# Performance work log

Measured on AMD Instinct MI355X. Metric: run time of the kernel, lower is better.

## Reference

```python
import jax, jax.numpy as jnp
import numpy as np

NB_HEAD = 16
SIZE_PER_HEAD = 64
D_MODEL = 1024
B, S = 4, 2048
NEG_BIG = 1e12  # matches the 1e12 additive-mask constant in the original


def setup_inputs() -> dict:
    key = jax.random.key(0)
    ks = jax.random.split(key, 8)
    Q_seq = jax.random.normal(ks[0], (B, S, D_MODEL), dtype=jnp.float32)
    K_seq = jax.random.normal(ks[1], (B, S, D_MODEL), dtype=jnp.float32)
    V_seq = jax.random.normal(ks[2], (B, S, D_MODEL), dtype=jnp.float32)
    out_dim = NB_HEAD * SIZE_PER_HEAD
    # glorot_uniform-style init
    lim = float(np.sqrt(6.0 / (D_MODEL + out_dim)))
    WQ = jax.random.uniform(ks[3], (D_MODEL, out_dim), minval=-lim, maxval=lim, dtype=jnp.float32)
    WK = jax.random.uniform(ks[4], (D_MODEL, out_dim), minval=-lim, maxval=lim, dtype=jnp.float32)
    WV = jax.random.uniform(ks[5], (D_MODEL, out_dim), minval=-lim, maxval=lim, dtype=jnp.float32)
    Q_len = jax.random.randint(ks[6], (B, 1), 1, S + 1, dtype=jnp.int32)
    V_len = jax.random.randint(ks[7], (B, 1), 1, S + 1, dtype=jnp.int32)
    return {"Q_seq": Q_seq, "K_seq": K_seq, "V_seq": V_seq,
            "WQ": WQ, "WK": WK, "WV": WV, "Q_len": Q_len, "V_len": V_len}


def _len_mask(lengths, seqlen, dtype):
    # one_hot(L) then 1 - cumsum along seq == (pos < L); L >= seqlen -> all ones
    return (jnp.arange(seqlen)[None, :] < lengths[:, 0][:, None]).astype(dtype)


def reference(Q_seq, K_seq, V_seq, WQ, WK, WV, Q_len, V_len):
    b, s, _ = Q_seq.shape
    h, dh = NB_HEAD, SIZE_PER_HEAD
    q = (Q_seq @ WQ).reshape(b, s, h, dh).transpose(0, 2, 1, 3)  # [B,H,S,Dh]
    k = (K_seq @ WK).reshape(b, s, h, dh).transpose(0, 2, 1, 3)
    v = (V_seq @ WV).reshape(b, s, h, dh).transpose(0, 2, 1, 3)
    scores = jnp.einsum('bhqd,bhkd->bhqk', q, k) / jnp.sqrt(jnp.float32(dh))
    mask_k = _len_mask(V_len, s, scores.dtype)  # [B,Sk]
    scores = scores - (1.0 - mask_k)[:, None, None, :] * NEG_BIG
    A = jax.nn.softmax(scores, axis=-1)
    o = jnp.einsum('bhqk,bhkd->bhqd', A, v)
    o = o.transpose(0, 2, 1, 3).reshape(b, s, h * dh)  # [B,S,D]
    mask_q = _len_mask(Q_len, s, o.dtype)
    return o * mask_q[:, :, None]
```

## Files before the change

kernel.cpp:

```cpp
#include <hip/hip_runtime.h>
#include <stdint.h>

typedef __attribute__((ext_vector_type(4))) float f32x4;
typedef __attribute__((ext_vector_type(8))) short bf16x8;
typedef __attribute__((ext_vector_type(4))) unsigned short u16x4;

#define MFMA16(a, b, c) __builtin_amdgcn_mfma_f32_16x16x32_bf16((a), (b), (c), 0, 0, 0)

static __device__ __forceinline__ unsigned short f2bf(float x) {
  union { float f; unsigned int u; } v; v.f = x;
  unsigned int r = v.u + 0x7fffu + ((v.u >> 16) & 1u);
  return (unsigned short)(r >> 16);
}

static __device__ __forceinline__ void gload_lds16(const void* g, void* l) {
  __builtin_amdgcn_global_load_lds(
      (__attribute__((address_space(1))) void*)(g),
      (__attribute__((address_space(3))) void*)(l), 16, 0, 0);
}

template <int CTRL>
static __device__ __forceinline__ float dpp_mov(float x) {
  union { float f; int i; } u, r;
  u.f = x;
  r.i = __builtin_amdgcn_update_dpp(u.i, u.i, CTRL, 0xF, 0xF, false);
  return r.f;
}
static __device__ __forceinline__ float dpp_max16(float x) {
  x = fmaxf(x, dpp_mov<0xB1>(x));
  x = fmaxf(x, dpp_mov<0x4E>(x));
  x = fmaxf(x, dpp_mov<0x124>(x));
  x = fmaxf(x, dpp_mov<0x128>(x));
  return x;
}
static __device__ __forceinline__ float dpp_sum16(float x) {
  x += dpp_mov<0xB1>(x);
  x += dpp_mov<0x4E>(x);
  x += dpp_mov<0x124>(x);
  x += dpp_mov<0x128>(x);
  return x;
}

__global__ void fill_kernel(float* p, int n, float v) {
  int i = blockIdx.x * blockDim.x + threadIdx.x;
  if (i < n) p[i] = v;
}

__global__ __launch_bounds__(256) void conv3_kernel(
    const float* __restrict__ S0, const float* __restrict__ S1, const float* __restrict__ S2,
    unsigned short* __restrict__ D0, unsigned short* __restrict__ D1,
    unsigned short* __restrict__ D2,
    const int* __restrict__ Qlen, const int* __restrict__ Vlen)
{
  const int y = blockIdx.y;
  {
    const int m0 = blockIdx.x * 4;
    const int b = m0 >> 11, s0 = m0 & 2047;
    const int L = (y == 0) ? Qlen[b] : Vlen[b];
    if (s0 >= ((L + 63) & ~63)) return;
  }
  const float* in = (y == 0) ? S0 : (y == 1) ? S1 : S2;
  unsigned short* outp = (y == 0) ? D0 : (y == 1) ? D1 : D2;
  const size_t base = ((size_t)blockIdx.x * 256 + threadIdx.x) * 16;
  const f32x4 a0 = *(const f32x4*)&in[base];
  const f32x4 a1 = *(const f32x4*)&in[base + 4];
  const f32x4 a2 = *(const f32x4*)&in[base + 8];
  const f32x4 a3 = *(const f32x4*)&in[base + 12];
  bf16x8 p0, p1;
#pragma unroll
  for (int u = 0; u < 4; ++u) {
    p0[u]     = (short)f2bf(a0[u]);
    p0[u + 4] = (short)f2bf(a1[u]);
    p1[u]     = (short)f2bf(a2[u]);
    p1[u + 4] = (short)f2bf(a3[u]);
  }
  *(bf16x8*)&outp[base]     = p0;
  *(bf16x8*)&outp[base + 8] = p1;
}

__global__ __launch_bounds__(256) void conv_kernel(
    const float* __restrict__ in, unsigned short* __restrict__ outp)
{
  const size_t base = ((size_t)blockIdx.x * 256 + threadIdx.x) * 16;
  const f32x4 a0 = *(const f32x4*)&in[base];
  const f32x4 a1 = *(const f32x4*)&in[base + 4];
  const f32x4 a2 = *(const f32x4*)&in[base + 8];
  const f32x4 a3 = *(const f32x4*)&in[base + 12];
  bf16x8 p0, p1;
#pragma unroll
  for (int u = 0; u < 4; ++u) {
    p0[u]     = (short)f2bf(a0[u]);
    p0[u + 4] = (short)f2bf(a1[u]);
    p1[u]     = (short)f2bf(a2[u]);
    p1[u + 4] = (short)f2bf(a3[u]);
  }
  *(bf16x8*)&outp[base]     = p0;
  *(bf16x8*)&outp[base + 8] = p1;
}

__global__ __launch_bounds__(256) void wtrans_kernel(
    const float* __restrict__ W0, const float* __restrict__ W1, const float* __restrict__ W2,
    unsigned short* __restrict__ T0, unsigned short* __restrict__ T1, unsigned short* __restrict__ T2)
{
  __shared__ __align__(16) float tile[64][65];
  const float* W = (blockIdx.z == 0) ? W0 : (blockIdx.z == 1) ? W1 : W2;
  unsigned short* T = (blockIdx.z == 0) ? T0 : (blockIdx.z == 1) ? T1 : T2;
  const int t = threadIdx.x;
  const int kb = blockIdx.x * 64, nb = blockIdx.y * 64;
  const int rr = t >> 4, cc = (t & 15) * 4;
#pragma unroll
  for (int p = 0; p < 4; ++p) {
    const int r = rr + p * 16;
    const f32x4 v = *(const f32x4*)&W[(size_t)(kb + r) * 1024 + nb + cc];
#pragma unroll
    for (int j = 0; j < 4; ++j) tile[r][cc + j] = v[j];
  }
  __syncthreads();
#pragma unroll
  for (int p = 0; p < 4; ++p) {
    const int n = rr + p * 16;
    u16x4 o;
#pragma unroll
    for (int j = 0; j < 4; ++j) o[j] = f2bf(tile[cc + j][n]);
    *(u16x4*)&T[(size_t)(nb + n) * 1024 + kb + cc] = o;
  }
}

__global__ __launch_bounds__(256) void proj_gemm_kernel(
    const unsigned short* __restrict__ A0, const unsigned short* __restrict__ A1,
    const unsigned short* __restrict__ A2,
    const unsigned short* __restrict__ B0, const unsigned short* __restrict__ B1,
    const unsigned short* __restrict__ B2,
    unsigned short* __restrict__ O0, unsigned short* __restrict__ O1,
    unsigned short* __restrict__ O2, int zbase,
    const int* __restrict__ Qlen, const int* __restrict__ Vlen)
{
  const int z = blockIdx.z + zbase;
  const int mm = (blockIdx.x + 8 * blockIdx.y + 24 * z) & 63;
  const int m0 = mm * 128, n0 = blockIdx.y * 128;

  int glim;
  {
    const int b = m0 >> 11, s0 = m0 & 2047;
    const int L = (z == 0) ? Qlen[b] : Vlen[b];
    const int C = (L + 63) & ~63;
    if (s0 >= C) return;
    glim = (m0 - s0) + C;
  }

  const unsigned short* Ab = (z == 0) ? A0 : (z == 1) ? A1 : A2;
  const unsigned short* Bt = (z == 0) ? B0 : (z == 1) ? B1 : B2;
  unsigned short* outp = (z == 0) ? O0 : (z == 1) ? O1 : O2;
  const float scale = (z == 0) ? 0.125f : 1.0f;

  __shared__ __align__(16) unsigned short Alds[4][128 * 32];
  __shared__ __align__(16) unsigned short Blds[4][128 * 32];
  const int t = threadIdx.x;
  const int lane = t & 63, w = t >> 6;
  const int wr = w >> 1, wc = w & 1;

  f32x4 acc[4][4] = {};

  const int L0 = t, L1 = t + 256;
  const int r0 = L0 >> 2, c0 = ((L0 & 3) ^ ((r0 >> 1) & 3)) * 8;
  const int r1 = L1 >> 2, c1 = ((L1 & 3) ^ ((r1 >> 1) & 3)) * 8;
  const int ra0 = min(m0 + r0, glim - 1);
  const int ra1 = min(m0 + r1, glim - 1);

#define PROJ_STAGE(tile, buf)                                                        \
  do {                                                                               \
    const int kt_ = (tile) * 32;                                                     \
    gload_lds16(&Ab[(size_t)ra0 * 1024 + kt_ + c0], &Alds[(buf)][L0 * 8]);           \
    gload_lds16(&Bt[(size_t)(n0 + r0) * 1024 + kt_ + c0], &Blds[(buf)][L0 * 8]);     \
    gload_lds16(&Ab[(size_t)ra1 * 1024 + kt_ + c1], &Alds[(buf)][L1 * 8]);           \
    gload_lds16(&Bt[(size_t)(n0 + r1) * 1024 + kt_ + c1], &Blds[(buf)][L1 * 8]);     \
  } while (0)

  PROJ_STAGE(0, 0);
  PROJ_STAGE(1, 1);
  PROJ_STAGE(2, 2);
  asm volatile("s_waitcnt vmcnt(8)" ::: "memory");
  __builtin_amdgcn_s_barrier();
  __builtin_amdgcn_sched_barrier(0);

  for (int tt = 0; tt < 32; ++tt) {
    const int cur = tt & 3;
    if (tt + 3 < 32) PROJ_STAGE(tt + 3, (tt + 3) & 3);

    const int q = lane >> 4;
    bf16x8 af[4], bfv[4];
#pragma unroll
    for (int m = 0; m < 4; ++m) {
      const int row = wr * 64 + m * 16 + (lane & 15);
      af[m] = *(const bf16x8*)&Alds[cur][row * 32 + ((q ^ ((row >> 1) & 3)) * 8)];
    }
#pragma unroll
    for (int n = 0; n < 4; ++n) {
      const int row = wc * 64 + n * 16 + (lane & 15);
      bfv[n] = *(const bf16x8*)&Blds[cur][row * 32 + ((q ^ ((row >> 1) & 3)) * 8)];
    }
    __builtin_amdgcn_s_setprio(1);
#pragma unroll
    for (int m = 0; m < 4; ++m)
#pragma unroll
      for (int n = 0; n < 4; ++n)
        acc[m][n] = MFMA16(af[m], bfv[n], acc[m][n]);
    __builtin_amdgcn_s_setprio(0);

    if (tt < 29)       asm volatile("s_waitcnt vmcnt(8)" ::: "memory");
    else if (tt == 29) asm volatile("s_waitcnt vmcnt(4)" ::: "memory");
    else               asm volatile("s_waitcnt vmcnt(0)" ::: "memory");
    __builtin_amdgcn_s_barrier();
    __builtin_amdgcn_sched_barrier(0);
  }
#undef PROJ_STAGE

#pragma unroll
  for (int mi = 0; mi < 4; ++mi) {
#pragma unroll
    for (int ni = 0; ni < 4; ++ni) {
      const int nn = n0 + wc * 64 + ni * 16 + (lane & 15);
      const int h = nn >> 6, d = nn & 63;
      const int mbase = m0 + wr * 64 + mi * 16 + ((lane >> 4) << 2);
      const int b = mbase >> 11;
      const int s = mbase & 2047;
      if (z != 2) {
#pragma unroll
        for (int j = 0; j < 4; ++j)
          outp[((size_t)(b * 16 + h) * 2048 + (s + j)) * 64 + d] = f2bf(acc[mi][ni][j] * scale);
      } else {
        u16x4 o;
#pragma unroll
        for (int j = 0; j < 4; ++j) o[j] = f2bf(acc[mi][ni][j]);
        *(u16x4*)&outp[((size_t)(b * 16 + h) * 64 + d) * 2048 + s] = o;
      }
    }
  }
}

__global__ __launch_bounds__(256) void attn_kernel(
    const unsigned short* __restrict__ qa, const unsigned short* __restrict__ ka,
    const unsigned short* __restrict__ va, const int* __restrict__ Qlen,
    const int* __restrict__ Vlen, float* __restrict__ outp)
{
  __shared__ __align__(16) unsigned char smem[36864];
  const int t = threadIdx.x, lane = t & 63, w = t >> 6;
  const int bh = blockIdx.y, b = bh >> 4, h = bh & 15;
  const int q0 = blockIdx.x * 16;
  const int Lq = Qlen[b], Lv = Vlen[b];
  float* outb = outp + (size_t)b * 2048 * 1024 + h * 64;

  if (q0 >= Lq) {
    const int r = t >> 4, c0 = (t & 15) * 4;
    const f32x4 z = {0.f, 0.f, 0.f, 0.f};
    *(f32x4*)&outb[(size_t)(q0 + r) * 1024 + c0] = z;
    return;
  }

  const unsigned short* qb = qa + (size_t)bh * 2048 * 64;
  const unsigned short* kb = ka + (size_t)bh * 2048 * 64;
  const unsigned short* vb = va + (size_t)bh * 64 * 2048;

  unsigned short* Klds = (unsigned short*)(smem + w * 9216);
  unsigned short* Vlds = (unsigned short*)(smem + w * 9216 + 4096);
  unsigned short* Plds = (unsigned short*)(smem + w * 9216 + 8192);

  bf16x8 aq[2];
  {
    const int qrow = q0 + (lane & 15);
#pragma unroll
    for (int f = 0; f < 2; ++f)
      aq[f] = *(const bf16x8*)&qb[(size_t)qrow * 64 + (lane >> 4) * 8 + f * 32];
  }

  float m_run[4], l_run[4];
  f32x4 acc_o[4] = {};
#pragma unroll
  for (int j = 0; j < 4; ++j) { m_run[j] = -3.0e38f; l_run[j] = 0.0f; }

  const int nt = (Lv + 31) >> 5;

  bf16x8 krg[4], vrg[4];
  int kt = w;
  if (kt < nt) {
    const int k0 = kt * 32;
#pragma unroll
    for (int i = 0; i < 4; ++i) {
      const int ci = lane + i * 64;
      krg[i] = *(const bf16x8*)&kb[(size_t)(k0 + (ci >> 3)) * 64 + (ci & 7) * 8];
      vrg[i] = *(const bf16x8*)&vb[(size_t)(ci >> 2) * 2048 + k0 + (ci & 3) * 8];
    }
#pragma unroll
    for (int i = 0; i < 4; ++i) {
      const int ci = lane + i * 64;
      const int kr = ci >> 3, kc = ci & 7;
      const int vr = ci >> 2, vc = ci & 3;
      *(bf16x8*)&Klds[kr * 64 + ((kc ^ (kr & 7)) * 8)] = krg[i];
      *(bf16x8*)&Vlds[vr * 32 + ((vc ^ (vr & 3)) * 8)] = vrg[i];
    }
  }

  for (; kt < nt; kt += 4) {
    const int k0 = kt * 32;
    const bool more = (kt + 4) < nt;
    if (more) {
      const int kn = k0 + 128;
#pragma unroll
      for (int i = 0; i < 4; ++i) {
        const int ci = lane + i * 64;
        krg[i] = *(const bf16x8*)&kb[(size_t)(kn + (ci >> 3)) * 64 + (ci & 7) * 8];
        vrg[i] = *(const bf16x8*)&vb[(size_t)(ci >> 2) * 2048 + kn + (ci & 3) * 8];
      }
    }

    f32x4 s4[2];
    __builtin_amdgcn_s_setprio(1);
#pragma unroll
    for (int kbk = 0; kbk < 2; ++kbk) {
      const int row = kbk * 16 + (lane & 15);
      f32x4 acc = {0.f, 0.f, 0.f, 0.f};
#pragma unroll
      for (int ds = 0; ds < 2; ++ds) {
        const int col = (((lane >> 4) * 8) + ds * 32) ^ ((row & 7) << 3);
        const bf16x8 bk = *(const bf16x8*)&Klds[row * 64 + col];
        acc = MFMA16(aq[ds], bk, acc);
      }
      if (k0 + row >= Lv) {
#pragma unroll
        for (int j = 0; j < 4; ++j) acc[j] = -1e30f;
      }
      s4[kbk] = acc;
    }
    __builtin_amdgcn_s_setprio(0);

    float mn[4], esc[4];
#pragma unroll
    for (int j = 0; j < 4; ++j) {
      float rm = fmaxf(s4[0][j], s4[1][j]);
      rm = dpp_max16(rm);
      mn[j] = fmaxf(m_run[j], rm);
      esc[j] = __expf(m_run[j] - mn[j]);
      m_run[j] = mn[j];
    }

    float p[2][4];
    float rs[4] = {0.f, 0.f, 0.f, 0.f};
#pragma unroll
    for (int kbk = 0; kbk < 2; ++kbk)
#pragma unroll
      for (int j = 0; j < 4; ++j) {
        p[kbk][j] = __expf(s4[kbk][j] - mn[j]);
        rs[j] += p[kbk][j];
      }

#pragma unroll
    for (int kbk = 0; kbk < 2; ++kbk)
#pragma unroll
      for (int j = 0; j < 4; ++j) {
        const int row = (lane >> 4) * 4 + j;
        const int pcol = kbk * 16 + (lane & 15);
        Plds[row * 32 + (((pcol >> 3) ^ (row & 3)) * 8) + (pcol & 7)] = f2bf(p[kbk][j]);
      }

#pragma unroll
    for (int j = 0; j < 4; ++j) {
      const float s = dpp_sum16(rs[j]);
      l_run[j] = l_run[j] * esc[j] + s;
    }
#pragma unroll
    for (int d = 0; d < 4; ++d)
#pragma unroll
      for (int j = 0; j < 4; ++j) acc_o[d][j] *= esc[j];

    bf16x8 pf;
    {
      const int row = lane & 15;
      pf = *(const bf16x8*)&Plds[row * 32 + (((lane >> 4) ^ (row & 3)) * 8)];
    }

    __builtin_amdgcn_s_setprio(1);
#pragma unroll
    for (int db = 0; db < 4; ++db) {
      const int vrow = db * 16 + (lane & 15);
      const int vch = (lane >> 4) ^ (vrow & 3);
      const bf16x8 vf = *(const bf16x8*)&Vlds[vrow * 32 + vch * 8];
      acc_o[db] = MFMA16(pf, vf, acc_o[db]);
    }
    __builtin_amdgcn_s_setprio(0);

    if (more) {
#pragma unroll
      for (int i = 0; i < 4; ++i) {
        const int ci = lane + i * 64;
        const int kr = ci >> 3, kc = ci & 7;
        const int vr = ci >> 2, vc = ci & 3;
        *(bf16x8*)&Klds[kr * 64 + ((kc ^ (kr & 7)) * 8)] = krg[i];
        *(bf16x8*)&Vlds[vr * 32 + ((vc ^ (vr & 3)) * 8)] = vrg[i];
      }
    }
  }

  __syncthreads();
  float* comb = (float*)smem;
  {
    float* my = comb + ((size_t)w * 64 + lane) * 24;
#pragma unroll
    for (int j = 0; j < 4; ++j) { my[j] = m_run[j]; my[4 + j] = l_run[j]; }
#pragma unroll
    for (int db = 0; db < 4; ++db)
#pragma unroll
      for (int j = 0; j < 4; ++j) my[8 + db * 4 + j] = acc_o[db][j];
  }
  __syncthreads();
  if (w == 0) {
#pragma unroll
    for (int ww = 1; ww < 4; ++ww) {
      const float* o = comb + ((size_t)ww * 64 + lane) * 24;
#pragma unroll
      for (int j = 0; j < 4; ++j) {
        const float mo = o[j];
        const float M = fmaxf(m_run[j], mo);
        const float e0 = __expf(m_run[j] - M);
        const float e1 = __expf(mo - M);
        l_run[j] = l_run[j] * e0 + o[4 + j] * e1;
#pragma unroll
        for (int db = 0; db < 4; ++db)
          acc_o[db][j] = acc_o[db][j] * e0 + o[8 + db * 4 + j] * e1;
        m_run[j] = M;
      }
    }
#pragma unroll
    for (int j = 0; j < 4; ++j) {
      const int row = q0 + (lane >> 4) * 4 + j;
      const float rl = 1.0f / l_run[j];
#pragma unroll
      for (int db = 0; db < 4; ++db) {
        const float v = acc_o[db][j] * rl;
        outb[(size_t)row * 1024 + db * 16 + (lane & 15)] = (row < Lq) ? v : 0.0f;
      }
    }
  }
}

extern "C" void kernel_launch(void* const* d_in, const int* in_sizes, int n_in,
                              void* d_out, int out_size, void* d_ws, size_t ws_size,
                              hipStream_t stream) {
  float* out = (float*)d_out;

  const float* Qs = (const float*)d_in[0];
  const float* Ks = (const float*)d_in[1];
  const float* Vs = (const float*)d_in[2];
  const float* WQ = (const float*)d_in[3];
  const float* WK = (const float*)d_in[4];
  const float* WV = (const float*)d_in[5];
  const int* Qlen = (const int*)d_in[6];
  const int* Vlen = (const int*)d_in[7];

  unsigned short* WQt = (unsigned short*)d_ws;
  unsigned short* WKt = WQt + (size_t)1024 * 1024;
  unsigned short* WVt = WKt + (size_t)1024 * 1024;
  unsigned short* qa  = WVt + (size_t)1024 * 1024;
  unsigned short* ka  = qa + (size_t)8192 * 1024;
  unsigned short* va  = ka + (size_t)8192 * 1024;
  unsigned short* ext = va + (size_t)8192 * 1024;

  unsigned short* cA = (unsigned short*)d_out;
  unsigned short* cB = cA + (size_t)8192 * 1024;

  const size_t base_need = ((size_t)3 * 1024 * 1024 + (size_t)3 * 8192 * 1024) * 2;
  const size_t ext_need  = base_need + (size_t)8192 * 1024 * 2;

  if (ws_size < base_need) {
    fill_kernel<<<(out_size + 255) / 256, 256, 0, stream>>>(out, out_size, 256.0f);
    return;
  }

  wtrans_kernel<<<dim3(16, 16, 3), 256, 0, stream>>>(WQ, WK, WV, WQt, WKt, WVt);

  if (ws_size >= ext_need) {
    conv3_kernel<<<dim3(2048, 3), 256, 0, stream>>>(Qs, Ks, Vs, cA, cB, ext, Qlen, Vlen);
    proj_gemm_kernel<<<dim3(64, 8, 3), 256, 0, stream>>>(
        cA, cB, ext, WQt, WKt, WVt, qa, ka, va, 0, Qlen, Vlen);
  } else {
    conv_kernel<<<2048, 256, 0, stream>>>(Qs, cA);
    conv_kernel<<<2048, 256, 0, stream>>>(Ks, cB);
    proj_gemm_kernel<<<dim3(64, 8, 2), 256, 0, stream>>>(
        cA, cB, cB, WQt, WKt, WVt, qa, ka, va, 0, Qlen, Vlen);
    conv_kernel<<<2048, 256, 0, stream>>>(Vs, cA);
    proj_gemm_kernel<<<dim3(64, 8, 1), 256, 0, stream>>>(
        cA, cA, cA, WQt, WKt, WVt, qa, ka, va, 2, Qlen, Vlen);
  }
  attn_kernel<<<dim3(128, 64), 256, 0, stream>>>(qa, ka, va, Qlen, Vlen, out);
}
```

Baseline: 120.7 us.

## Process four 16-row query groups per attention block to reuse K/V tiles

Each attention block now handles 64 query rows (four 16-row groups) instead of 16, so every K/V tile loaded into LDS feeds four groups of MFMA work. The grid shrinks to a quarter. This cuts redundant global K/V traffic and per-tile load overhead. In exchange, register pressure rises because Q fragments, running max/sum and output accumulators are quadrupled. The cross-wave combine now runs four times with extra barriers, and the coarser query granularity skips less work for short Q lengths.

```diff
diff --git a/kernel.cpp b/kernel.cpp
--- a/kernel.cpp
+++ b/kernel.cpp
@@ -246,14 +246,17 @@
   __shared__ __align__(16) unsigned char smem[36864];
   const int t = threadIdx.x, lane = t & 63, w = t >> 6;
   const int bh = blockIdx.y, b = bh >> 4, h = bh & 15;
-  const int q0 = blockIdx.x * 16;
+  const int q0 = blockIdx.x * 64;
   const int Lq = Qlen[b], Lv = Vlen[b];
   float* outb = outp + (size_t)b * 2048 * 1024 + h * 64;
 
   if (q0 >= Lq) {
-    const int r = t >> 4, c0 = (t & 15) * 4;
-    const f32x4 z = {0.f, 0.f, 0.f, 0.f};
-    *(f32x4*)&outb[(size_t)(q0 + r) * 1024 + c0] = z;
+    const int r = t >> 2, c0 = (t & 3) * 16;
+#pragma unroll
+    for (int j = 0; j < 4; ++j) {
+      const f32x4 z = {0.f, 0.f, 0.f, 0.f};
+      *(f32x4*)&outb[(size_t)(q0 + r) * 1024 + c0 + j * 4] = z;
+    }
     return;
   }
 
@@ -265,18 +268,21 @@
   unsigned short* Vlds = (unsigned short*)(smem + w * 9216 + 4096);
   unsigned short* Plds = (unsigned short*)(smem + w * 9216 + 8192);
 
-  bf16x8 aq[2];
-  {
-    const int qrow = q0 + (lane & 15);
+  bf16x8 aq[4][2];
+#pragma unroll
+  for (int g = 0; g < 4; ++g) {
+    const int qrow = q0 + g * 16 + (lane & 15);
 #pragma unroll
     for (int f = 0; f < 2; ++f)
-      aq[f] = *(const bf16x8*)&qb[(size_t)qrow * 64 + (lane >> 4) * 8 + f * 32];
-  }
-
-  float m_run[4], l_run[4];
-  f32x4 acc_o[4] = {};
-#pragma unroll
-  for (int j = 0; j < 4; ++j) { m_run[j] = -3.0e38f; l_run[j] = 0.0f; }
+      aq[g][f] = *(const bf16x8*)&qb[(size_t)qrow * 64 + (lane >> 4) * 8 + f * 32];
+  }
+
+  float m_run[4][4], l_run[4][4];
+  f32x4 acc_o[4][4] = {};
+#pragma unroll
+  for (int g = 0; g < 4; ++g)
+#pragma unroll
+    for (int j = 0; j < 4; ++j) { m_run[g][j] = -3.0e38f; l_run[g][j] = 0.0f; }
 
   const int nt = (Lv + 31) >> 5;
 
@@ -313,80 +319,83 @@
       }
     }
 
-    f32x4 s4[2];
-    __builtin_amdgcn_s_setprio(1);
-#pragma unroll
-    for (int kbk = 0; kbk < 2; ++kbk) {
-      const int row = kbk * 16 + (lane & 15);
-      f32x4 acc = {0.f, 0.f, 0.f, 0.f};
-#pragma unroll
-      for (int ds = 0; ds < 2; ++ds) {
-        const int col = (((lane >> 4) * 8) + ds * 32) ^ ((row & 7) << 3);
-        const bf16x8 bk = *(const bf16x8*)&Klds[row * 64 + col];
-        acc = MFMA16(aq[ds], bk, acc);
-      }
-      if (k0 + row >= Lv) {
-#pragma unroll
-        for (int j = 0; j < 4; ++j) acc[j] = -1e30f;
-      }
-      s4[kbk] = acc;
-    }
-    __builtin_amdgcn_s_setprio(0);
-
-    float mn[4], esc[4];
-#pragma unroll
-    for (int j = 0; j < 4; ++j) {
-      float rm = fmaxf(s4[0][j], s4[1][j]);
-      rm = dpp_max16(rm);
-      mn[j] = fmaxf(m_run[j], rm);
-      esc[j] = __expf(m_run[j] - mn[j]);
-      m_run[j] = mn[j];
-    }
-
-    float p[2][4];
-    float rs[4] = {0.f, 0.f, 0.f, 0.f};
-#pragma unroll
-    for (int kbk = 0; kbk < 2; ++kbk)
+#pragma unroll
+    for (int g = 0; g < 4; ++g) {
+      f32x4 s4[2];
+      __builtin_amdgcn_s_setprio(1);
+#pragma unroll
+      for (int kbk = 0; kbk < 2; ++kbk) {
+        const int row = kbk * 16 + (lane & 15);
+        f32x4 acc = {0.f, 0.f, 0.f, 0.f};
+#pragma unroll
+        for (int ds = 0; ds < 2; ++ds) {
+          const int col = (((lane >> 4) * 8) + ds * 32) ^ ((row & 7) << 3);
+          const bf16x8 bk = *(const bf16x8*)&Klds[row * 64 + col];
+          acc = MFMA16(aq[g][ds], bk, acc);
+        }
+        if (k0 + row >= Lv) {
+#pragma unroll
+          for (int j = 0; j < 4; ++j) acc[j] = -1e30f;
+        }
+        s4[kbk] = acc;
+      }
+      __builtin_amdgcn_s_setprio(0);
+
+      float mn[4], esc[4];
 #pragma unroll
       for (int j = 0; j < 4; ++j) {
-        p[kbk][j] = __expf(s4[kbk][j] - mn[j]);
-        rs[j] += p[kbk][j];
-      }
-
-#pragma unroll
-    for (int kbk = 0; kbk < 2; ++kbk)
+        float rm = fmaxf(s4[0][j], s4[1][j]);
+        rm = dpp_max16(rm);
+        mn[j] = fmaxf(m_run[g][j], rm);
+        esc[j] = __expf(m_run[g][j] - mn[j]);
+        m_run[g][j] = mn[j];
+      }
+
+      float p[2][4];
+      float rs[4] = {0.f, 0.f, 0.f, 0.f};
+#pragma unroll
+      for (int kbk = 0; kbk < 2; ++kbk)
+#pragma unroll
+        for (int j = 0; j < 4; ++j) {
+          p[kbk][j] = __expf(s4[kbk][j] - mn[j]);
+          rs[j] += p[kbk][j];
+        }
+
+#pragma unroll
+      for (int kbk = 0; kbk < 2; ++kbk)
+#pragma unroll
+        for (int j = 0; j < 4; ++j) {
+          const int row = (lane >> 4) * 4 + j;
+          const int pcol = kbk * 16 + (lane & 15);
+          Plds[row * 32 + (((pcol >> 3) ^ (row & 3)) * 8) + (pcol & 7)] = f2bf(p[kbk][j]);
+        }
+
 #pragma unroll
       for (int j = 0; j < 4; ++j) {
-        const int row = (lane >> 4) * 4 + j;
-        const int pcol = kbk * 16 + (lane & 15);
-        Plds[row * 32 + (((pcol >> 3) ^ (row & 3)) * 8) + (pcol & 7)] = f2bf(p[kbk][j]);
-      }
-
-#pragma unroll
-    for (int j = 0; j < 4; ++j) {
-      const float s = dpp_sum16(rs[j]);
-      l_run[j] = l_run[j] * esc[j] + s;
-    }
-#pragma unroll
-    for (int d = 0; d < 4; ++d)
-#pragma unroll
-      for (int j = 0; j < 4; ++j) acc_o[d][j] *= esc[j];
-
-    bf16x8 pf;
-    {
-      const int row = lane & 15;
-      pf = *(const bf16x8*)&Plds[row * 32 + (((lane >> 4) ^ (row & 3)) * 8)];
-    }
-
-    __builtin_amdgcn_s_setprio(1);
-#pragma unroll
-    for (int db = 0; db < 4; ++db) {
-      const int vrow = db * 16 + (lane & 15);
-      const int vch = (lane >> 4) ^ (vrow & 3);
-      const bf16x8 vf = *(const bf16x8*)&Vlds[vrow * 32 + vch * 8];
-      acc_o[db] = MFMA16(pf, vf, acc_o[db]);
-    }
-    __builtin_amdgcn_s_setprio(0);
+        const float s = dpp_sum16(rs[j]);
+        l_run[g][j] = l_run[g][j] * esc[j] + s;
+      }
+#pragma unroll
+      for (int d = 0; d < 4; ++d)
+#pragma unroll
+        for (int j = 0; j < 4; ++j) acc_o[g][d][j] *= esc[j];
+
+      bf16x8 pf;
+      {
+        const int row = lane & 15;
+        pf = *(const bf16x8*)&Plds[row * 32 + (((lane >> 4) ^ (row & 3)) * 8)];
+      }
+
+      __builtin_amdgcn_s_setprio(1);
+#pragma unroll
+      for (int db = 0; db < 4; ++db) {
+        const int vrow = db * 16 + (lane & 15);
+        const int vch = (lane >> 4) ^ (vrow & 3);
+        const bf16x8 vf = *(const bf16x8*)&Vlds[vrow * 32 + vch * 8];
+        acc_o[g][db] = MFMA16(pf, vf, acc_o[g][db]);
+      }
+      __builtin_amdgcn_s_setprio(0);
+    }
 
     if (more) {
 #pragma unroll
@@ -400,43 +409,52 @@
     }
   }
 
-  __syncthreads();
   float* comb = (float*)smem;
-  {
-    float* my = comb + ((size_t)w * 64 + lane) * 24;
-#pragma unroll
-    for (int j = 0; j < 4; ++j) { my[j] = m_run[j]; my[4 + j] = l_run[j]; }
-#pragma unroll
-    for (int db = 0; db < 4; ++db)
-#pragma unroll
-      for (int j = 0; j < 4; ++j) my[8 + db * 4 + j] = acc_o[db][j];
-  }
-  __syncthreads();
-  if (w == 0) {
-#pragma unroll
-    for (int ww = 1; ww < 4; ++ww) {
-      const float* o = comb + ((size_t)ww * 64 + lane) * 24;
+#pragma unroll
+  for (int g = 0; g < 4; ++g) {
+    __syncthreads();
+    {
+      float* my = comb + ((size_t)w * 64 + lane) * 24;
+#pragma unroll
+      for (int j = 0; j < 4; ++j) { my[j] = m_run[g][j]; my[4 + j] = l_run[g][j]; }
+#pragma unroll
+      for (int db = 0; db < 4; ++db)
+#pragma unroll
+        for (int j = 0; j < 4; ++j) my[8 + db * 4 + j] = acc_o[g][db][j];
+    }
+    __syncthreads();
+    if (w == 0) {
+      float mg[4], lg[4];
+      f32x4 ag[4];
+#pragma unroll
+      for (int j = 0; j < 4; ++j) { mg[j] = m_run[g][j]; lg[j] = l_run[g][j]; }
+#pragma unroll
+      for (int db = 0; db < 4; ++db) ag[db] = acc_o[g][db];
+#pragma unroll
+      for (int ww = 1; ww < 4; ++ww) {
+        const float* o = comb + ((size_t)ww * 64 + lane) * 24;
+#pragma unroll
+        for (int j = 0; j < 4; ++j) {
+          const float mo = o[j];
+          const float M = fmaxf(mg[j], mo);
+          const float e0 = __expf(mg[j] - M);
+          const float e1 = __expf(mo - M);
+          lg[j] = lg[j] * e0 + o[4 + j] * e1;
+#pragma unroll
+          for (int db = 0; db < 4; ++db)
+            ag[db][j] = ag[db][j] * e0 + o[8 + db * 4 + j] * e1;
+          mg[j] = M;
+        }
+      }
 #pragma unroll
       for (int j = 0; j < 4; ++j) {
-        const float mo = o[j];
-        const float M = fmaxf(m_run[j], mo);
-        const float e0 = __expf(m_run[j] - M);
-        const float e1 = __expf(mo - M);
-        l_run[j] = l_run[j] * e0 + o[4 + j] * e1;
-#pragma unroll
-        for (int db = 0; db < 4; ++db)
-          acc_o[db][j] = acc_o[db][j] * e0 + o[8 + db * 4 + j] * e1;
-        m_run[j] = M;
-      }
-    }
-#pragma unroll
-    for (int j = 0; j < 4; ++j) {
-      const int row = q0 + (lane >> 4) * 4 + j;
-      const float rl = 1.0f / l_run[j];
-#pragma unroll
-      for (int db = 0; db < 4; ++db) {
-        const float v = acc_o[db][j] * rl;
-        outb[(size_t)row * 1024 + db * 16 + (lane & 15)] = (row < Lq) ? v : 0.0f;
+        const int row = q0 + g * 16 + (lane >> 4) * 4 + j;
+        const float rl = 1.0f / lg[j];
+#pragma unroll
+        for (int db = 0; db < 4; ++db) {
+          const float v = ag[db][j] * rl;
+          outb[(size_t)row * 1024 + db * 16 + (lane & 15)] = (row < Lq) ? v : 0.0f;
+        }
       }
     }
   }
@@ -490,5 +508,5 @@
     proj_gemm_kernel<<<dim3(64, 8, 1), 256, 0, stream>>>(
         cA, cA, cA, WQt, WKt, WVt, qa, ka, va, 2, Qlen, Vlen);
   }
-  attn_kernel<<<dim3(128, 64), 256, 0, stream>>>(qa, ka, va, Qlen, Vlen, out);
-}
+  attn_kernel<<<dim3(32, 64), 256, 0, stream>>>(qa, ka, va, Qlen, Vlen, out);
+}
```

After: 234.0 us. +93.8%, slower.
